# Optimization experiments

Measured on AMD Instinct MI355X. Metric: run time of the kernel, lower is better.

## Reference

```python
import jax, jax.numpy as jnp
import numpy as np

B, S, T, H, V = 32, 64, 64, 512, 32000


def setup_inputs() -> dict:
    key = jax.random.key(0)
    ks = jax.random.split(key, 14)
    enc = jax.random.normal(ks[0], (B, S, H), jnp.float32)
    h0 = jax.random.normal(ks[1], (1, B, H), jnp.float32)
    # encoder padding mask: at least half of each row valid (avoids all -inf rows)
    src_len = jax.random.randint(ks[2], (B,), S // 2, S + 1)
    enc_mask = (jnp.arange(S)[None, :] < src_len[:, None])
    tgt = jax.random.randint(ks[3], (B, T), 0, V)
    fra_len = jax.random.randint(ks[4], (B,), 1, T + 1).at[0].set(T)
    s = 1.0 / np.sqrt(H)
    emb = jax.random.normal(ks[5], (V, H), jnp.float32) * s
    W_ih = jax.random.uniform(ks[6], (3 * H, H), jnp.float32, -s, s)
    W_hh = jax.random.uniform(ks[7], (3 * H, H), jnp.float32, -s, s)
    b_ih = jax.random.uniform(ks[8], (3 * H,), jnp.float32, -s, s)
    b_hh = jax.random.uniform(ks[9], (3 * H,), jnp.float32, -s, s)
    W_cc = jax.random.uniform(ks[10], (H, 2 * H), jnp.float32, -s, s)
    b_cc = jnp.zeros((H,), jnp.float32)
    W_out = jax.random.uniform(ks[11], (V, H), jnp.float32, -s, s)
    b_out = jnp.zeros((V,), jnp.float32)
    return {"all_encoder_hidden_states": enc, "initial_decoder_hidden_state": h0,
            "encoder_output_mask": enc_mask, "target_input": tgt, "fra_length": fra_len,
            "embedding": emb, "W_ih": W_ih, "W_hh": W_hh, "b_ih": b_ih, "b_hh": b_hh,
            "W_cc": W_cc, "b_cc": b_cc, "W_out": W_out, "b_out": b_out}


def reference(all_encoder_hidden_states, initial_decoder_hidden_state, encoder_output_mask,
              target_input, fra_length, embedding, W_ih, W_hh, b_ih, b_hh,
              W_cc, b_cc, W_out, b_out):
    enc = all_encoder_hidden_states            # [B,S,H]
    mask = encoder_output_mask                 # [B,S] bool
    xs = embedding[target_input].transpose(1, 0, 2)  # [T,B,H]
    ts = jnp.arange(xs.shape[0])

    def step(h, inp):                          # h: [B,H]
        x, t = inp
        gx = x @ W_ih.T + b_ih                 # [B,3H]
        gh = h @ W_hh.T + b_hh
        gxr, gxz, gxn = jnp.split(gx, 3, axis=-1)
        ghr, ghz, ghn = jnp.split(gh, 3, axis=-1)
        r = jax.nn.sigmoid(gxr + ghr)
        z = jax.nn.sigmoid(gxz + ghz)
        n = jnp.tanh(gxn + r * ghn)
        h_new = (1.0 - z) * n + z * h          # torch GRU update
        # Luong dot-product attention
        scores = jnp.einsum('bsh,bh->bs', enc, h_new)
        scores = jnp.where(mask, scores, -jnp.inf)
        alphas = jax.nn.softmax(scores, axis=-1)
        ctx = jnp.einsum('bs,bsh->bh', alphas, enc)
        ho = jnp.tanh(jnp.concatenate([ctx, h_new], axis=-1) @ W_cc.T + b_cc)
        logit = ho @ W_out.T + b_out           # [B,V]
        active = (t < fra_length)[:, None]
        h_next = jnp.where(active, h_new, h)   # freeze finished sequences
        return h_next, logit

    _, logits = jax.lax.scan(step, initial_decoder_hidden_state[0], (xs, ts))
    logits = logits.transpose(1, 0, 2)          # [B,T,V]
    return jax.nn.log_softmax(logits, axis=-1)
```

## Files before the change

### kernel.cpp

```cpp
#include <hip/hip_runtime.h>

static constexpr int Bn = 32, Sn = 64, Tn = 64, Hn = 512, Vn = 32000;
static constexpr int H3 = 1536;

typedef __attribute__((ext_vector_type(8))) short bf16x8;
typedef __attribute__((ext_vector_type(4))) float f32x4;

__device__ __forceinline__ short f2bf(float f) {
    unsigned u = __float_as_uint(f);
    u += 0x7FFFu + ((u >> 16) & 1u);
    return (short)(u >> 16);
}
__device__ __forceinline__ float bf2f(short s) {
    return __uint_as_float(((unsigned)(unsigned short)s) << 16);
}

__device__ __forceinline__ void gload16(const void* g, void* l) {
    __builtin_amdgcn_global_load_lds(
        (const __attribute__((address_space(1))) unsigned int*)g,
        (__attribute__((address_space(3))) unsigned int*)l, 16, 0, 0);
}

__global__ __launch_bounds__(256) void k_prep(const int* __restrict__ tgt,
                                              const float* __restrict__ emb,
                                              const float* __restrict__ W_ih,
                                              const float* __restrict__ W_hh,
                                              const float* __restrict__ W_cc,
                                              short* __restrict__ Xb,
                                              short* __restrict__ Wih_b, short* __restrict__ Whh_b,
                                              short* __restrict__ Wc1_b, short* __restrict__ Wc2_b) {
    const int bid = blockIdx.x, tid = threadIdx.x;
    if (bid < 2048) {
        long u = (long)bid * 256 + tid;
        const float* src; short* dst;
        if (u < 196608)       { long e = u * 4;            src = W_ih + e; dst = Wih_b + e; }
        else if (u < 393216)  { long e = (u - 196608) * 4; src = W_hh + e; dst = Whh_b + e; }
        else if (u < 458752)  { long e = (u - 393216) * 4; long r = e >> 9; int c = (int)(e & 511);
                                src = W_cc + r * 1024 + c;       dst = Wc1_b + e; }
        else                  { long e = (u - 458752) * 4; long r = e >> 9; int c = (int)(e & 511);
                                src = W_cc + r * 1024 + 512 + c; dst = Wc2_b + e; }
        const float4 v = *(const float4*)src;
        short4 o; o.x = f2bf(v.x); o.y = f2bf(v.y); o.z = f2bf(v.z); o.w = f2bf(v.w);
        *(short4*)dst = o;
    } else {
        const int m = (bid - 2048) * 2 + (tid >> 7);
        const int c = (tid & 127) * 4;
        const float4 v = *(const float4*)(emb + (long)tgt[m] * Hn + c);
        short4 o; o.x = f2bf(v.x); o.y = f2bf(v.y); o.z = f2bf(v.z); o.w = f2bf(v.w);
        *(short4*)(Xb + (long)m * Hn + c) = o;
    }
}

__global__ __launch_bounds__(256) void k_gemm_bf16(const short* __restrict__ A, int lda,
                                                   const short* __restrict__ Bm, int ldb,
                                                   const float* __restrict__ bias,
                                                   float* __restrict__ C, int ldc, int K) {
    __shared__ short lA[4096];
    __shared__ short lB[4096];
    const int tid = threadIdx.x;
    const int row0 = blockIdx.y * 128;
    const int col0 = blockIdx.x * 128;
    const int lane = tid & 63;
    const int w = tid >> 6;
    const int wr = w >> 1, wc = w & 1;
    const int g = lane >> 4, rr = lane & 15;

    f32x4 acc[4][4];
    for (int m = 0; m < 4; ++m)
        for (int n = 0; n < 4; ++n)
            for (int q = 0; q < 4; ++q) acc[m][n][q] = 0.f;

    for (int kk = 0; kk < K; kk += 32) {
        for (int p = 0; p < 2; ++p) {
            int u = p * 256 + tid;
            int kg = u >> 7, r = u & 127;
            gload16(A + (long)(row0 + r) * lda + kk + kg * 8, &lA[u * 8]);
            gload16(Bm + (long)(col0 + r) * ldb + kk + kg * 8, &lB[u * 8]);
        }
        __syncthreads();
        bf16x8 av[4], bv[4];
        for (int m = 0; m < 4; ++m)
            av[m] = *(const bf16x8*)&lA[(g * 128 + wr * 64 + m * 16 + rr) * 8];
        for (int n = 0; n < 4; ++n)
            bv[n] = *(const bf16x8*)&lB[(g * 128 + wc * 64 + n * 16 + rr) * 8];
        for (int m = 0; m < 4; ++m)
            for (int n = 0; n < 4; ++n)
                acc[m][n] = __builtin_amdgcn_mfma_f32_16x16x32_bf16(av[m], bv[n], acc[m][n], 0, 0, 0);
        __syncthreads();
    }

    for (int n = 0; n < 4; ++n) {
        int gc = col0 + wc * 64 + n * 16 + rr;
        float bb = bias ? bias[gc] : 0.f;
        for (int m = 0; m < 4; ++m) {
            int gr = row0 + wr * 64 + m * 16 + g * 4;
            for (int q = 0; q < 4; ++q)
                C[(long)(gr + q) * ldc + gc] = acc[m][n][q] + bb;
        }
    }
}

__global__ __launch_bounds__(256) void k_gemm_logits(const short* __restrict__ A,
                                                     const short* __restrict__ Bm,
                                                     const float* __restrict__ bias,
                                                     float* __restrict__ Cf,
                                                     short* __restrict__ Cb,
                                                     float* __restrict__ stats,
                                                     int use_bf16) {
    __shared__ short lA[4096];
    __shared__ short lB[4096];
    __shared__ float sml[128][2];
    __shared__ float ssl[128][2];
    const int tid = threadIdx.x;
    const int row0 = blockIdx.y * 128;
    const int col0 = blockIdx.x * 128;
    const int lane = tid & 63;
    const int w = tid >> 6;
    const int wr = w >> 1, wc = w & 1;
    const int g = lane >> 4, rr = lane & 15;

    f32x4 acc[4][4];
    for (int m = 0; m < 4; ++m)
        for (int n = 0; n < 4; ++n)
            for (int q = 0; q < 4; ++q) acc[m][n][q] = 0.f;

    for (int kk = 0; kk < 512; kk += 32) {
        for (int p = 0; p < 2; ++p) {
            int u = p * 256 + tid;
            int kg = u >> 7, r = u & 127;
            gload16(A + (long)(row0 + r) * 512 + kk + kg * 8, &lA[u * 8]);
            gload16(Bm + (long)(col0 + r) * 512 + kk + kg * 8, &lB[u * 8]);
        }
        __syncthreads();
        bf16x8 av[4], bv[4];
        for (int m = 0; m < 4; ++m)
            av[m] = *(const bf16x8*)&lA[(g * 128 + wr * 64 + m * 16 + rr) * 8];
        for (int n = 0; n < 4; ++n)
            bv[n] = *(const bf16x8*)&lB[(g * 128 + wc * 64 + n * 16 + rr) * 8];
        for (int m = 0; m < 4; ++m)
            for (int n = 0; n < 4; ++n)
                acc[m][n] = __builtin_amdgcn_mfma_f32_16x16x32_bf16(av[m], bv[n], acc[m][n], 0, 0, 0);
        __syncthreads();
    }

    float bb[4];
    #pragma unroll
    for (int n = 0; n < 4; ++n) bb[n] = bias[col0 + wc * 64 + n * 16 + rr];

    if (use_bf16) {
        #pragma unroll
        for (int n = 0; n < 4; ++n) {
            int gc = col0 + wc * 64 + n * 16 + rr;
            #pragma unroll
            for (int m = 0; m < 4; ++m) {
                int gr = row0 + wr * 64 + m * 16 + g * 4;
                #pragma unroll
                for (int q = 0; q < 4; ++q)
                    Cb[(long)(gr + q) * Vn + gc] = f2bf(acc[m][n][q] + bb[n]);
            }
        }
    } else {
        #pragma unroll
        for (int n = 0; n < 4; ++n) {
            int gc = col0 + wc * 64 + n * 16 + rr;
            #pragma unroll
            for (int m = 0; m < 4; ++m) {
                int gr = row0 + wr * 64 + m * 16 + g * 4;
                #pragma unroll
                for (int q = 0; q < 4; ++q)
                    Cf[(long)(gr + q) * Vn + gc] = acc[m][n][q] + bb[n];
            }
        }
    }
    #pragma unroll
    for (int m = 0; m < 4; ++m) {
        #pragma unroll
        for (int q = 0; q < 4; ++q) {
            float mx = acc[m][0][q] + bb[0];
            mx = fmaxf(mx, acc[m][1][q] + bb[1]);
            mx = fmaxf(mx, acc[m][2][q] + bb[2]);
            mx = fmaxf(mx, acc[m][3][q] + bb[3]);
            mx = fmaxf(mx, __shfl_xor(mx, 1));
            mx = fmaxf(mx, __shfl_xor(mx, 2));
            mx = fmaxf(mx, __shfl_xor(mx, 4));
            mx = fmaxf(mx, __shfl_xor(mx, 8));
            float s = __expf(acc[m][0][q] + bb[0] - mx) + __expf(acc[m][1][q] + bb[1] - mx)
                    + __expf(acc[m][2][q] + bb[2] - mx) + __expf(acc[m][3][q] + bb[3] - mx);
            s += __shfl_xor(s, 1);
            s += __shfl_xor(s, 2);
            s += __shfl_xor(s, 4);
            s += __shfl_xor(s, 8);
            if (rr == 0) {
                const int r = wr * 64 + m * 16 + g * 4 + q;
                sml[r][wc] = mx; ssl[r][wc] = s;
            }
        }
    }
    __syncthreads();
    if (tid < 128) {
        const float m0 = sml[tid][0], m1 = sml[tid][1];
        const float mm = fmaxf(m0, m1);
        const float ss = ssl[tid][0] * __expf(m0 - mm) + ssl[tid][1] * __expf(m1 - mm);
        float2* sp = (float2*)stats;
        sp[(long)(row0 + tid) * 256 + blockIdx.x] = make_float2(mm, ss);
    }
}

__global__ __launch_bounds__(256) void k_sub(float* __restrict__ out, const short* __restrict__ Cb,
                                             const float* __restrict__ stats, int use_bf16) {
    const long row = blockIdx.x;
    const int tid = threadIdx.x;
    __shared__ float lse_s;
    if (tid < 64) {
        float m = -__builtin_inff(), s = 0.f;
        for (int tc = tid; tc < 250; tc += 64) {
            const float2 p = ((const float2*)stats)[row * 256 + tc];
            const float nm = fmaxf(m, p.x);
            s = s * __expf(m - nm) + p.y * __expf(p.x - nm);
            m = nm;
        }
        for (int o = 1; o < 64; o <<= 1) {
            const float om = __shfl_xor(m, o), os = __shfl_xor(s, o);
            const float nm = fmaxf(m, om);
            s = s * __expf(m - nm) + os * __expf(om - nm);
            m = nm;
        }
        if (tid == 0) lse_s = m + logf(s);
    }
    __syncthreads();
    const float lse = lse_s;
    float* p = out + row * (long)Vn;
    if (use_bf16) {
        const short* cp = Cb + row * (long)Vn;
        for (int i = tid; i < Vn / 4; i += 256) {
            short4 c = *(const short4*)(cp + i * 4);
            float4 v;
            v.x = bf2f(c.x) - lse; v.y = bf2f(c.y) - lse;
            v.z = bf2f(c.z) - lse; v.w = bf2f(c.w) - lse;
            *(float4*)(p + i * 4) = v;
        }
    } else {
        for (int i = tid; i < Vn / 4; i += 256) {
            float4 v = *(const float4*)(p + i * 4);
            v.x -= lse; v.y -= lse; v.z -= lse; v.w -= lse;
            *(float4*)(p + i * 4) = v;
        }
    }
}

__global__ __launch_bounds__(256) void k_ho(const short* __restrict__ A1, const short* __restrict__ A2,
                                            const short* __restrict__ B1, const short* __restrict__ B2,
                                            const float* __restrict__ bias, short* __restrict__ C) {
    __shared__ short lA[4096];
    __shared__ short lB[4096];
    const int tid = threadIdx.x;
    const int row0 = blockIdx.y * 128;
    const int col0 = blockIdx.x * 128;
    const int lane = tid & 63;
    const int w = tid >> 6;
    const int wr = w >> 1, wc = w & 1;
    const int g = lane >> 4, rr = lane & 15;

    f32x4 acc[4][4];
    for (int m = 0; m < 4; ++m)
        for (int n = 0; n < 4; ++n)
            for (int q = 0; q < 4; ++q) acc[m][n][q] = 0.f;

    for (int ph = 0; ph < 2; ++ph) {
        const short* A = ph ? A2 : A1;
        const short* Bm = ph ? B2 : B1;
        for (int kk = 0; kk < 512; kk += 32) {
            for (int p = 0; p < 2; ++p) {
                int u = p * 256 + tid;
                int kg = u >> 7, r = u & 127;
                gload16(A + (long)(row0 + r) * 512 + kk + kg * 8, &lA[u * 8]);
                gload16(Bm + (long)(col0 + r) * 512 + kk + kg * 8, &lB[u * 8]);
            }
            __syncthreads();
            bf16x8 av[4], bv[4];
            for (int m = 0; m < 4; ++m)
                av[m] = *(const bf16x8*)&lA[(g * 128 + wr * 64 + m * 16 + rr) * 8];
            for (int n = 0; n < 4; ++n)
                bv[n] = *(const bf16x8*)&lB[(g * 128 + wc * 64 + n * 16 + rr) * 8];
            for (int m = 0; m < 4; ++m)
                for (int n = 0; n < 4; ++n)
                    acc[m][n] = __builtin_amdgcn_mfma_f32_16x16x32_bf16(av[m], bv[n], acc[m][n], 0, 0, 0);
            __syncthreads();
        }
    }

    for (int n = 0; n < 4; ++n) {
        int gc = col0 + wc * 64 + n * 16 + rr;
        float bb = bias[gc];
        for (int m = 0; m < 4; ++m) {
            int gr = row0 + wr * 64 + m * 16 + g * 4;
            for (int q = 0; q < 4; ++q)
                C[(long)(gr + q) * 512 + gc] = f2bf(tanhf(acc[m][n][q] + bb));
        }
    }
}

__device__ __forceinline__ void sig_flag(unsigned* slot, unsigned val) {
    asm volatile("s_waitcnt vmcnt(0)" ::: "memory");
    __syncthreads();
    if (threadIdx.x == 0)
        __hip_atomic_store(slot, val, __ATOMIC_RELAXED, __HIP_MEMORY_SCOPE_AGENT);
}

__global__ __launch_bounds__(512, 1) void k_seq(
    const float* __restrict__ GX, const int* __restrict__ fra,
    const float* __restrict__ h0,
    const short* __restrict__ Whh_b, const float* __restrict__ b_hh,
    short* __restrict__ hn_all,
    unsigned long long* __restrict__ hn_pub,
    unsigned* __restrict__ flags,
    const float* __restrict__ W_out, short* __restrict__ Wout_b)
{
    __shared__ __align__(16) short h_all[Bn * Hn];
    __shared__ float gh_sl[3 * 16 * 32];
    const int bid = blockIdx.x;
    const int tid = threadIdx.x;

    if (bid >= Bn) {
        const long base = (long)(bid - Bn) * (512 * 16);
        #pragma unroll
        for (int it = 0; it < 16; ++it) {
            long i = base + it * 512 + tid;
            if (i < (long)Vn * Hn / 4) {
                const float4 v = *(const float4*)(W_out + i * 4);
                short4 o; o.x = f2bf(v.x); o.y = f2bf(v.y); o.z = f2bf(v.z); o.w = f2bf(v.w);
                *(short4*)(Wout_b + i * 4) = o;
            }
        }
        return;
    }

    const int wv = tid >> 6, lane = tid & 63;
    bf16x8 afr[16];
    if (wv < 6) {
        const int g = wv >> 1;
        const int row = g * 512 + bid * 16 + (lane & 15);
        #pragma unroll
        for (int k = 0; k < 16; ++k)
            afr[k] = *(const bf16x8*)(Whh_b + (long)row * 512 + k * 32 + (lane >> 4) * 8);
    }
    #pragma unroll
    for (int it = 0; it < 8; ++it) {
        const int idx2 = it * 512 + tid;
        const int b = idx2 >> 7, ci2 = idx2 & 127;
        const int j0 = ci2 * 4;
        const int soff = b * 512 + ((((ci2 >> 1)) ^ (b & 7)) << 3) + (ci2 & 1) * 4;
        const float4 v = *(const float4*)(h0 + b * 512 + j0);
        unsigned long long pk = (unsigned long long)(unsigned short)f2bf(v.x)
                              | ((unsigned long long)(unsigned short)f2bf(v.y) << 16)
                              | ((unsigned long long)(unsigned short)f2bf(v.z) << 32)
                              | ((unsigned long long)(unsigned short)f2bf(v.w) << 48);
        *(unsigned long long*)&h_all[soff] = pk;
    }

    const int eb = tid >> 4, jj = tid & 15;
    float h_carry = h0[eb * 512 + bid * 16 + jj];
    const int flen_e = fra[eb];
    const int jglob = bid * 16 + jj;
    const float bhr = b_hh[jglob];
    const float bhz = b_hh[512 + jglob];
    const float bhn = b_hh[1024 + jglob];

    const int ci2s = wv * 16 + (lane & 15);
    const unsigned* fp = flags + (ci2s >> 2) * 32;
    const int bbase = lane >> 4;

    for (int t = 0; t < Tn; ++t) {
        const long base = (long)(eb * Tn + t) * H3 + jglob;
        const float gxr = GX[base];
        const float gxz = GX[base + 512];
        const float gxn = GX[base + 1024];
        if (t >= 1) {
            while (__hip_atomic_load(fp, __ATOMIC_RELAXED, __HIP_MEMORY_SCOPE_AGENT) < (unsigned)t)
                __builtin_amdgcn_s_sleep(1);
            const unsigned long long* src = hn_pub + ((t - 1) & 1) * 4096;
            #pragma unroll
            for (int it = 0; it < 8; ++it) {
                const int b = bbase + it * 4;
                const unsigned long long v =
                    __hip_atomic_load(src + b * 128 + ci2s, __ATOMIC_RELAXED, __HIP_MEMORY_SCOPE_AGENT);
                const int soff = b * 512 + ((((ci2s >> 1)) ^ (b & 7)) << 3) + (ci2s & 1) * 4;
                *(unsigned long long*)&h_all[soff] = v;
            }
        }
        __syncthreads();
        if (wv < 6) {
            const int g = wv >> 1, n = wv & 1;
            const int bq = n * 16 + (lane & 15);
            f32x4 a0 = {0.f, 0.f, 0.f, 0.f}, a1 = {0.f, 0.f, 0.f, 0.f};
            #pragma unroll
            for (int k = 0; k < 8; ++k) {
                const int c0 = k * 4 + (lane >> 4);
                const int c1 = (k + 8) * 4 + (lane >> 4);
                bf16x8 b0 = *(const bf16x8*)&h_all[bq * 512 + ((c0 ^ (bq & 7)) << 3)];
                bf16x8 b1 = *(const bf16x8*)&h_all[bq * 512 + ((c1 ^ (bq & 7)) << 3)];
                a0 = __builtin_amdgcn_mfma_f32_16x16x32_bf16(afr[k], b0, a0, 0, 0, 0);
                a1 = __builtin_amdgcn_mfma_f32_16x16x32_bf16(afr[k + 8], b1, a1, 0, 0, 0);
            }
            const int r0 = (lane >> 4) * 4;
            #pragma unroll
            for (int q = 0; q < 4; ++q)
                gh_sl[g * 512 + (r0 + q) * 32 + bq] = a0[q] + a1[q];
        }
        __syncthreads();
        {
            const float ghr = gh_sl[jj * 32 + eb]          + bhr;
            const float ghz = gh_sl[512 + jj * 32 + eb]    + bhz;
            const float ghn = gh_sl[1024 + jj * 32 + eb]   + bhn;
            const float r = 1.f / (1.f + __expf(-(gxr + ghr)));
            const float z = 1.f / (1.f + __expf(-(gxz + ghz)));
            const float nn = tanhf(gxn + r * ghn);
            const float hv = (1.f - z) * nn + z * h_carry;
            h_carry = (t < flen_e) ? hv : h_carry;
            int w32 = (int)(unsigned short)f2bf(h_carry);
            int n1 = __shfl_down(w32, 1);
            int n2 = __shfl_down(w32, 2);
            int n3 = __shfl_down(w32, 3);
            if ((jj & 3) == 0) {
                unsigned long long pk = (unsigned long long)(unsigned)(w32 | (n1 << 16))
                                      | ((unsigned long long)(unsigned)(n2 | (n3 << 16)) << 32);
                __hip_atomic_store(hn_pub + (t & 1) * 4096 + eb * 128 + bid * 4 + (jj >> 2), pk,
                                   __ATOMIC_RELAXED, __HIP_MEMORY_SCOPE_AGENT);
            }
            sig_flag(flags + bid * 32, (unsigned)(t + 1));
            hn_all[(long)(eb * Tn + t) * Hn + jglob] = f2bf(hv);
        }
    }
}

__global__ __launch_bounds__(512, 1) void k_attn(
    const float* __restrict__ enc, const short* __restrict__ hn_all,
    const void* __restrict__ maskp, short* __restrict__ ctx_b)
{
    __shared__ __align__(16) short encl[64 * 536];
    __shared__ __align__(16) short hnlbuf[64 * 536];
    __shared__ __align__(16) float scl[64 * 64];
    __shared__ __align__(16) short albc[64 * 72];
    const int b = blockIdx.x;
    const int tid = threadIdx.x;
    const int wv = tid >> 6, lane = tid & 63;
    const int g = lane >> 4, rr = lane & 15;

    const unsigned w0 = ((const unsigned*)maskp)[0];
    const int mmode = (w0 == 1u) ? 0 : (w0 == 0x3F800000u ? 2 : 1);

    {
        const float* encb = enc + (long)b * (Sn * Hn);
        #pragma unroll
        for (int it = 0; it < 16; ++it) {
            int e = (it * 512 + tid) * 4;
            float4 v = *(const float4*)(encb + e);
            int s = e >> 9, k = e & 511;
            short4 o; o.x = f2bf(v.x); o.y = f2bf(v.y); o.z = f2bf(v.z); o.w = f2bf(v.w);
            *(short4*)(encl + s * 536 + k) = o;
        }
    }
    {
        const short* hb = hn_all + (long)b * (Tn * Hn);
        #pragma unroll
        for (int it = 0; it < 8; ++it) {
            int u = it * 512 + tid;
            int t = u >> 6, k8 = (u & 63) * 8;
            *(int4*)(hnlbuf + t * 536 + k8) = *(const int4*)(hb + t * 512 + k8);
        }
    }
    __syncthreads();

    for (int i = 0; i < 2; ++i) {
        const int id = wv * 2 + i;
        const int tt = id >> 2, ss = id & 3;
        f32x4 a0 = {0.f, 0.f, 0.f, 0.f}, a1 = {0.f, 0.f, 0.f, 0.f};
        #pragma unroll
        for (int k = 0; k < 8; ++k) {
            bf16x8 av0 = *(const bf16x8*)&hnlbuf[(tt * 16 + rr) * 536 + k * 32 + g * 8];
            bf16x8 bv0 = *(const bf16x8*)&encl[(ss * 16 + rr) * 536 + k * 32 + g * 8];
            bf16x8 av1 = *(const bf16x8*)&hnlbuf[(tt * 16 + rr) * 536 + (k + 8) * 32 + g * 8];
            bf16x8 bv1 = *(const bf16x8*)&encl[(ss * 16 + rr) * 536 + (k + 8) * 32 + g * 8];
            a0 = __builtin_amdgcn_mfma_f32_16x16x32_bf16(av0, bv0, a0, 0, 0, 0);
            a1 = __builtin_amdgcn_mfma_f32_16x16x32_bf16(av1, bv1, a1, 0, 0, 0);
        }
        #pragma unroll
        for (int q = 0; q < 4; ++q)
            scl[(tt * 16 + g * 4 + q) * 64 + ss * 16 + rr] = a0[q] + a1[q];
    }
    __syncthreads();

    {
        const int t = wv * 8 + (lane >> 3);
        const int sub = lane & 7;
        float v[8];
        #pragma unroll
        for (int e = 0; e < 8; ++e) {
            const int s = sub * 8 + e;
            bool mv;
            if (mmode == 0)      mv = ((const int*)maskp)[b * Sn + s] != 0;
            else if (mmode == 1) mv = ((const unsigned char*)maskp)[b * Sn + s] != 0;
            else                 mv = ((const float*)maskp)[b * Sn + s] != 0.f;
            v[e] = mv ? scl[t * 64 + s] : -__builtin_inff();
        }
        float mx = v[0];
        #pragma unroll
        for (int e = 1; e < 8; ++e) mx = fmaxf(mx, v[e]);
        mx = fmaxf(mx, __shfl_xor(mx, 1));
        mx = fmaxf(mx, __shfl_xor(mx, 2));
        mx = fmaxf(mx, __shfl_xor(mx, 4));
        float su = 0.f;
        float ev[8];
        #pragma unroll
        for (int e = 0; e < 8; ++e) { ev[e] = __expf(v[e] - mx); su += ev[e]; }
        su += __shfl_xor(su, 1);
        su += __shfl_xor(su, 2);
        su += __shfl_xor(su, 4);
        const float inv = 1.f / su;
        bf16x8 o;
        #pragma unroll
        for (int e = 0; e < 8; ++e) o[e] = f2bf(ev[e] * inv);
        *(bf16x8*)&albc[t * 72 + sub * 8] = o;
    }
    {
        short* enct = hnlbuf;
        const int j = tid;
        #pragma unroll
        for (int c = 0; c < 8; ++c) {
            bf16x8 tmp;
            #pragma unroll
            for (int e = 0; e < 8; ++e) tmp[e] = encl[(c * 8 + e) * 536 + j];
            *(bf16x8*)&enct[j * 64 + ((c ^ (j & 7)) * 8)] = tmp;
        }
    }
    __syncthreads();

    {
        const short* enct = hnlbuf;
        for (int i = 0; i < 16; ++i) {
            const int id = wv * 16 + i;
            const int tt = id >> 5, jt = id & 31;
            const int jr = jt * 16 + rr;
            f32x4 acc = {0.f, 0.f, 0.f, 0.f};
            #pragma unroll
            for (int kk = 0; kk < 2; ++kk) {
                bf16x8 av = *(const bf16x8*)&albc[(tt * 16 + rr) * 72 + kk * 32 + g * 8];
                const int c = kk * 4 + g;
                bf16x8 bv = *(const bf16x8*)&enct[jr * 64 + ((c ^ (jr & 7)) * 8)];
                acc = __builtin_amdgcn_mfma_f32_16x16x32_bf16(av, bv, acc, 0, 0, 0);
            }
            #pragma unroll
            for (int q = 0; q < 4; ++q) {
                const int t = tt * 16 + g * 4 + q;
                ctx_b[(long)(b * Tn + t) * Hn + jr] = f2bf(acc[q]);
            }
        }
    }
}

extern "C" void kernel_launch(void* const* d_in, const int* in_sizes, int n_in,
                              void* d_out, int out_size, void* d_ws, size_t ws_size,
                              hipStream_t stream) {
    const float* enc   = (const float*)d_in[0];
    const float* h0    = (const float*)d_in[1];
    const void*  maskp = d_in[2];
    const int*   tgt   = (const int*)d_in[3];
    const int*   fra   = (const int*)d_in[4];
    const float* emb   = (const float*)d_in[5];
    const float* W_ih  = (const float*)d_in[6];
    const float* W_hh  = (const float*)d_in[7];
    const float* b_ih  = (const float*)d_in[8];
    const float* b_hh  = (const float*)d_in[9];
    const float* W_cc  = (const float*)d_in[10];
    const float* b_cc  = (const float*)d_in[11];
    const float* W_out = (const float*)d_in[12];
    const float* b_out = (const float*)d_in[13];
    float* out = (float*)d_out;

    char* ws = (char*)d_ws;
    float*    GX      = (float*)ws;   ws += (long)2048 * 1536 * 4;
    short*    Xb      = (short*)ws;   ws += (long)2048 * 512 * 2;
    short*    Wih_b   = (short*)ws;   ws += (long)1536 * 512 * 2;
    short*    Wout_b  = (short*)ws;   ws += (long)32000 * 512 * 2;
    short*    Whh_b   = (short*)ws;   ws += (long)1536 * 512 * 2;
    short*    Wc1_b   = (short*)ws;   ws += (long)512 * 512 * 2;
    short*    Wcc2_b  = (short*)ws;   ws += (long)512 * 512 * 2;
    short*    ho_b    = (short*)ws;   ws += (long)2048 * 512 * 2;
    short*    hn_all  = (short*)ws;   ws += (long)2048 * 512 * 2;
    short*    ctx_b   = (short*)ws;   ws += (long)2048 * 512 * 2;
    float*    stats   = (float*)ws;   ws += (long)2048 * 256 * 2 * 4;
    unsigned long long* hn_pub = (unsigned long long*)ws; ws += (long)2 * 4096 * 8;
    unsigned* flags   = (unsigned*)ws; ws += 1024 * 4;
    const long cb_bytes = (long)2048 * Vn * 2;
    const long used = (long)(ws - (char*)d_ws);
    const int use_bf16 = (ws_size >= (size_t)(used + cb_bytes)) ? 1 : 0;
    short* Cb = use_bf16 ? (short*)ws : nullptr;

    hipMemsetAsync(flags, 0, 1024 * 4, stream);
    k_prep<<<3072, 256, 0, stream>>>(tgt, emb, W_ih, W_hh, W_cc, Xb, Wih_b, Whh_b, Wc1_b, Wcc2_b);

    k_gemm_bf16<<<dim3(12, 16), 256, 0, stream>>>(Xb, 512, Wih_b, 512, b_ih, GX, 1536, 512);

    k_seq<<<544, 512, 0, stream>>>(GX, fra, h0, Whh_b, b_hh, hn_all, hn_pub, flags, W_out, Wout_b);

    k_attn<<<32, 512, 0, stream>>>(enc, hn_all, maskp, ctx_b);

    k_ho<<<dim3(4, 16), 256, 0, stream>>>(ctx_b, hn_all, Wc1_b, Wcc2_b, b_cc, ho_b);

    k_gemm_logits<<<dim3(250, 16), 256, 0, stream>>>(ho_b, Wout_b, b_out, out, Cb, stats, use_bf16);

    k_sub<<<2048, 256, 0, stream>>>(out, Cb, stats, use_bf16);
}
```

Baseline: 675.1 us.

## Fuse attention into sequential GRU kernel via flag-driven consumer blocks

```diff
diff --git a/kernel.cpp b/kernel.cpp
--- a/kernel.cpp
+++ b/kernel.cpp
@@ -300,29 +300,49 @@
     }
 }
 
+struct WSm3 {
+    short h_all[Bn * Hn];
+    float gh_sl[3 * 16 * 32];
+};
+struct ASm3 {
+    short encl[Sn * 520];
+    float scp[8][64];
+    float al[64];
+    short hnf[Hn];
+};
+union USm3 { WSm3 w; ASm3 a; };
+
 __device__ __forceinline__ void sig_flag(unsigned* slot, unsigned val) {
     asm volatile("s_waitcnt vmcnt(0)" ::: "memory");
     __syncthreads();
     if (threadIdx.x == 0)
         __hip_atomic_store(slot, val, __ATOMIC_RELAXED, __HIP_MEMORY_SCOPE_AGENT);
 }
+__device__ __forceinline__ void wait_flags32(const unsigned* base, unsigned need) {
+    if (threadIdx.x < 32) {
+        while (__hip_atomic_load(base + threadIdx.x * 32, __ATOMIC_RELAXED, __HIP_MEMORY_SCOPE_AGENT) < need)
+            __builtin_amdgcn_s_sleep(1);
+    }
+    __syncthreads();
+}
 
 __global__ __launch_bounds__(512, 1) void k_seq(
     const float* __restrict__ GX, const int* __restrict__ fra,
     const float* __restrict__ h0,
     const short* __restrict__ Whh_b, const float* __restrict__ b_hh,
-    short* __restrict__ hn_all,
+    const float* __restrict__ enc, const void* __restrict__ maskp,
+    unsigned long long* __restrict__ hn_pk,
+    short* __restrict__ ctx_b,
     unsigned long long* __restrict__ hn_pub,
     unsigned* __restrict__ flags,
     const float* __restrict__ W_out, short* __restrict__ Wout_b)
 {
-    __shared__ __align__(16) short h_all[Bn * Hn];
-    __shared__ float gh_sl[3 * 16 * 32];
+    __shared__ __align__(16) USm3 sm;
     const int bid = blockIdx.x;
     const int tid = threadIdx.x;
 
-    if (bid >= Bn) {
-        const long base = (long)(bid - Bn) * (512 * 16);
+    if (bid >= 64) {
+        const long base = (long)(bid - 64) * (512 * 16);
         #pragma unroll
         for (int it = 0; it < 16; ++it) {
             long i = base + it * 512 + tid;
@@ -336,6 +356,75 @@
     }
 
     const int wv = tid >> 6, lane = tid & 63;
+
+    if (bid >= Bn) {
+        const int b = bid - Bn;
+        const unsigned w0 = ((const unsigned*)maskp)[0];
+        const int mmode = (w0 == 1u) ? 0 : (w0 == 0x3F800000u ? 2 : 1);
+        {
+            const float* encb = enc + (long)b * (Sn * Hn);
+            #pragma unroll
+            for (int it = 0; it < 16; ++it) {
+                int e = (it * 512 + tid) * 4;
+                float4 v = *(const float4*)(encb + e);
+                int s = e >> 9, k = e & 511;
+                short4 o; o.x = f2bf(v.x); o.y = f2bf(v.y); o.z = f2bf(v.z); o.w = f2bf(v.w);
+                *(short4*)(sm.a.encl + s * 520 + k) = o;
+            }
+        }
+        __syncthreads();
+        for (int u = 0; u < Tn; ++u) {
+            wait_flags32(flags, (unsigned)(u + 1));
+            if (tid < 128) {
+                unsigned long long v = __hip_atomic_load(hn_pk + (long)(b * Tn + u) * 128 + tid,
+                                                         __ATOMIC_RELAXED, __HIP_MEMORY_SCOPE_AGENT);
+                *(unsigned long long*)&sm.a.hnf[tid * 4] = v;
+            }
+            __syncthreads();
+            {
+                const int s = tid & 63, sub = tid >> 6;
+                const short* erow = sm.a.encl + s * 520 + sub * 64;
+                const short* hrow = sm.a.hnf + sub * 64;
+                float p = 0.f;
+                #pragma unroll
+                for (int c8 = 0; c8 < 8; ++c8) {
+                    bf16x8 ev = *(const bf16x8*)(erow + c8 * 8);
+                    bf16x8 hv8 = *(const bf16x8*)(hrow + c8 * 8);
+                    #pragma unroll
+                    for (int e = 0; e < 8; ++e)
+                        p += bf2f(ev[e]) * bf2f(hv8[e]);
+                }
+                sm.a.scp[sub][s] = p;
+            }
+            __syncthreads();
+            if (tid < 64) {
+                float v = 0.f;
+                #pragma unroll
+                for (int q = 0; q < 8; ++q) v += sm.a.scp[q][tid];
+                bool mv;
+                if (mmode == 0)      mv = ((const int*)maskp)[b * Sn + tid] != 0;
+                else if (mmode == 1) mv = ((const unsigned char*)maskp)[b * Sn + tid] != 0;
+                else                 mv = ((const float*)maskp)[b * Sn + tid] != 0.f;
+                v = mv ? v : -__builtin_inff();
+                float mx = v;
+                for (int o = 1; o < 64; o <<= 1) mx = fmaxf(mx, __shfl_xor(mx, o));
+                float e = __expf(v - mx);
+                float su = e;
+                for (int o = 1; o < 64; o <<= 1) su += __shfl_xor(su, o);
+                sm.a.al[tid] = e / su;
+            }
+            __syncthreads();
+            {
+                float cx = 0.f;
+                #pragma unroll 8
+                for (int s = 0; s < 64; ++s)
+                    cx += sm.a.al[s] * bf2f(sm.a.encl[s * 520 + tid]);
+                ctx_b[(long)(b * Tn + u) * Hn + tid] = f2bf(cx);
+            }
+        }
+        return;
+    }
+
     bf16x8 afr[16];
     if (wv < 6) {
         const int g = wv >> 1;
@@ -355,7 +444,7 @@
                               | ((unsigned long long)(unsigned short)f2bf(v.y) << 16)
                               | ((unsigned long long)(unsigned short)f2bf(v.z) << 32)
                               | ((unsigned long long)(unsigned short)f2bf(v.w) << 48);
-        *(unsigned long long*)&h_all[soff] = pk;
+        *(unsigned long long*)&sm.w.h_all[soff] = pk;
     }
 
     const int eb = tid >> 4, jj = tid & 15;
@@ -385,7 +474,7 @@
                 const unsigned long long v =
                     __hip_atomic_load(src + b * 128 + ci2s, __ATOMIC_RELAXED, __HIP_MEMORY_SCOPE_AGENT);
                 const int soff = b * 512 + ((((ci2s >> 1)) ^ (b & 7)) << 3) + (ci2s & 1) * 4;
-                *(unsigned long long*)&h_all[soff] = v;
+                *(unsigned long long*)&sm.w.h_all[soff] = v;
             }
         }
         __syncthreads();
@@ -397,163 +486,41 @@
             for (int k = 0; k < 8; ++k) {
                 const int c0 = k * 4 + (lane >> 4);
                 const int c1 = (k + 8) * 4 + (lane >> 4);
-                bf16x8 b0 = *(const bf16x8*)&h_all[bq * 512 + ((c0 ^ (bq & 7)) << 3)];
-                bf16x8 b1 = *(const bf16x8*)&h_all[bq * 512 + ((c1 ^ (bq & 7)) << 3)];
+                bf16x8 b0 = *(const bf16x8*)&sm.w.h_all[bq * 512 + ((c0 ^ (bq & 7)) << 3)];
+                bf16x8 b1 = *(const bf16x8*)&sm.w.h_all[bq * 512 + ((c1 ^ (bq & 7)) << 3)];
                 a0 = __builtin_amdgcn_mfma_f32_16x16x32_bf16(afr[k], b0, a0, 0, 0, 0);
                 a1 = __builtin_amdgcn_mfma_f32_16x16x32_bf16(afr[k + 8], b1, a1, 0, 0, 0);
             }
             const int r0 = (lane >> 4) * 4;
             #pragma unroll
             for (int q = 0; q < 4; ++q)
-                gh_sl[g * 512 + (r0 + q) * 32 + bq] = a0[q] + a1[q];
+                sm.w.gh_sl[g * 512 + (r0 + q) * 32 + bq] = a0[q] + a1[q];
         }
         __syncthreads();
         {
-            const float ghr = gh_sl[jj * 32 + eb]          + bhr;
-            const float ghz = gh_sl[512 + jj * 32 + eb]    + bhz;
-            const float ghn = gh_sl[1024 + jj * 32 + eb]   + bhn;
+            const float ghr = sm.w.gh_sl[jj * 32 + eb]          + bhr;
+            const float ghz = sm.w.gh_sl[512 + jj * 32 + eb]    + bhz;
+            const float ghn = sm.w.gh_sl[1024 + jj * 32 + eb]   + bhn;
             const float r = 1.f / (1.f + __expf(-(gxr + ghr)));
             const float z = 1.f / (1.f + __expf(-(gxz + ghz)));
             const float nn = tanhf(gxn + r * ghn);
             const float hv = (1.f - z) * nn + z * h_carry;
             h_carry = (t < flen_e) ? hv : h_carry;
-            int w32 = (int)(unsigned short)f2bf(h_carry);
-            int n1 = __shfl_down(w32, 1);
-            int n2 = __shfl_down(w32, 2);
-            int n3 = __shfl_down(w32, 3);
+            int f32w = (int)(unsigned short)f2bf(h_carry);
+            int r32w = (int)(unsigned short)f2bf(hv);
+            int f1 = __shfl_down(f32w, 1), f2 = __shfl_down(f32w, 2), f3 = __shfl_down(f32w, 3);
+            int r1 = __shfl_down(r32w, 1), r2 = __shfl_down(r32w, 2), r3 = __shfl_down(r32w, 3);
             if ((jj & 3) == 0) {
-                unsigned long long pk = (unsigned long long)(unsigned)(w32 | (n1 << 16))
-                                      | ((unsigned long long)(unsigned)(n2 | (n3 << 16)) << 32);
-                __hip_atomic_store(hn_pub + (t & 1) * 4096 + eb * 128 + bid * 4 + (jj >> 2), pk,
+                unsigned long long pkf = (unsigned long long)(unsigned)(f32w | (f1 << 16))
+                                       | ((unsigned long long)(unsigned)(f2 | (f3 << 16)) << 32);
+                unsigned long long pkr = (unsigned long long)(unsigned)(r32w | (r1 << 16))
+                                       | ((unsigned long long)(unsigned)(r2 | (r3 << 16)) << 32);
+                __hip_atomic_store(hn_pub + (t & 1) * 4096 + eb * 128 + bid * 4 + (jj >> 2), pkf,
                                    __ATOMIC_RELAXED, __HIP_MEMORY_SCOPE_AGENT);
+                __hip_atomic_store(hn_pk + (long)(eb * Tn + t) * 128 + bid * 4 + (jj >> 2), pkr,
+                                   __ATOMIC_RELAXED, __HIP_MEMORY_SCOPE_AGENT);
             }
             sig_flag(flags + bid * 32, (unsigned)(t + 1));
-            hn_all[(long)(eb * Tn + t) * Hn + jglob] = f2bf(hv);
-        }
-    }
-}
-
-__global__ __launch_bounds__(512, 1) void k_attn(
-    const float* __restrict__ enc, const short* __restrict__ hn_all,
-    const void* __restrict__ maskp, short* __restrict__ ctx_b)
-{
-    __shared__ __align__(16) short encl[64 * 536];
-    __shared__ __align__(16) short hnlbuf[64 * 536];
-    __shared__ __align__(16) float scl[64 * 64];
-    __shared__ __align__(16) short albc[64 * 72];
-    const int b = blockIdx.x;
-    const int tid = threadIdx.x;
-    const int wv = tid >> 6, lane = tid & 63;
-    const int g = lane >> 4, rr = lane & 15;
-
-    const unsigned w0 = ((const unsigned*)maskp)[0];
-    const int mmode = (w0 == 1u) ? 0 : (w0 == 0x3F800000u ? 2 : 1);
-
-    {
-        const float* encb = enc + (long)b * (Sn * Hn);
-        #pragma unroll
-        for (int it = 0; it < 16; ++it) {
-            int e = (it * 512 + tid) * 4;
-            float4 v = *(const float4*)(encb + e);
-            int s = e >> 9, k = e & 511;
-            short4 o; o.x = f2bf(v.x); o.y = f2bf(v.y); o.z = f2bf(v.z); o.w = f2bf(v.w);
-            *(short4*)(encl + s * 536 + k) = o;
-        }
-    }
-    {
-        const short* hb = hn_all + (long)b * (Tn * Hn);
-        #pragma unroll
-        for (int it = 0; it < 8; ++it) {
-            int u = it * 512 + tid;
-            int t = u >> 6, k8 = (u & 63) * 8;
-            *(int4*)(hnlbuf + t * 536 + k8) = *(const int4*)(hb + t * 512 + k8);
-        }
-    }
-    __syncthreads();
-
-    for (int i = 0; i < 2; ++i) {
-        const int id = wv * 2 + i;
-        const int tt = id >> 2, ss = id & 3;
-        f32x4 a0 = {0.f, 0.f, 0.f, 0.f}, a1 = {0.f, 0.f, 0.f, 0.f};
-        #pragma unroll
-        for (int k = 0; k < 8; ++k) {
-            bf16x8 av0 = *(const bf16x8*)&hnlbuf[(tt * 16 + rr) * 536 + k * 32 + g * 8];
-            bf16x8 bv0 = *(const bf16x8*)&encl[(ss * 16 + rr) * 536 + k * 32 + g * 8];
-            bf16x8 av1 = *(const bf16x8*)&hnlbuf[(tt * 16 + rr) * 536 + (k + 8) * 32 + g * 8];
-            bf16x8 bv1 = *(const bf16x8*)&encl[(ss * 16 + rr) * 536 + (k + 8) * 32 + g * 8];
-            a0 = __builtin_amdgcn_mfma_f32_16x16x32_bf16(av0, bv0, a0, 0, 0, 0);
-            a1 = __builtin_amdgcn_mfma_f32_16x16x32_bf16(av1, bv1, a1, 0, 0, 0);
-        }
-        #pragma unroll
-        for (int q = 0; q < 4; ++q)
-            scl[(tt * 16 + g * 4 + q) * 64 + ss * 16 + rr] = a0[q] + a1[q];
-    }
-    __syncthreads();
-
-    {
-        const int t = wv * 8 + (lane >> 3);
-        const int sub = lane & 7;
-        float v[8];
-        #pragma unroll
-        for (int e = 0; e < 8; ++e) {
-            const int s = sub * 8 + e;
-            bool mv;
-            if (mmode == 0)      mv = ((const int*)maskp)[b * Sn + s] != 0;
-            else if (mmode == 1) mv = ((const unsigned char*)maskp)[b * Sn + s] != 0;
-            else                 mv = ((const float*)maskp)[b * Sn + s] != 0.f;
-            v[e] = mv ? scl[t * 64 + s] : -__builtin_inff();
-        }
-        float mx = v[0];
-        #pragma unroll
-        for (int e = 1; e < 8; ++e) mx = fmaxf(mx, v[e]);
-        mx = fmaxf(mx, __shfl_xor(mx, 1));
-        mx = fmaxf(mx, __shfl_xor(mx, 2));
-        mx = fmaxf(mx, __shfl_xor(mx, 4));
-        float su = 0.f;
-        float ev[8];
-        #pragma unroll
-        for (int e = 0; e < 8; ++e) { ev[e] = __expf(v[e] - mx); su += ev[e]; }
-        su += __shfl_xor(su, 1);
-        su += __shfl_xor(su, 2);
-        su += __shfl_xor(su, 4);
-        const float inv = 1.f / su;
-        bf16x8 o;
-        #pragma unroll
-        for (int e = 0; e < 8; ++e) o[e] = f2bf(ev[e] * inv);
-        *(bf16x8*)&albc[t * 72 + sub * 8] = o;
-    }
-    {
-        short* enct = hnlbuf;
-        const int j = tid;
-        #pragma unroll
-        for (int c = 0; c < 8; ++c) {
-            bf16x8 tmp;
-            #pragma unroll
-            for (int e = 0; e < 8; ++e) tmp[e] = encl[(c * 8 + e) * 536 + j];
-            *(bf16x8*)&enct[j * 64 + ((c ^ (j & 7)) * 8)] = tmp;
-        }
-    }
-    __syncthreads();
-
-    {
-        const short* enct = hnlbuf;
-        for (int i = 0; i < 16; ++i) {
-            const int id = wv * 16 + i;
-            const int tt = id >> 5, jt = id & 31;
-            const int jr = jt * 16 + rr;
-            f32x4 acc = {0.f, 0.f, 0.f, 0.f};
-            #pragma unroll
-            for (int kk = 0; kk < 2; ++kk) {
-                bf16x8 av = *(const bf16x8*)&albc[(tt * 16 + rr) * 72 + kk * 32 + g * 8];
-                const int c = kk * 4 + g;
-                bf16x8 bv = *(const bf16x8*)&enct[jr * 64 + ((c ^ (jr & 7)) * 8)];
-                acc = __builtin_amdgcn_mfma_f32_16x16x32_bf16(av, bv, acc, 0, 0, 0);
-            }
-            #pragma unroll
-            for (int q = 0; q < 4; ++q) {
-                const int t = tt * 16 + g * 4 + q;
-                ctx_b[(long)(b * Tn + t) * Hn + jr] = f2bf(acc[q]);
-            }
         }
     }
 }
@@ -601,9 +568,9 @@
 
     k_gemm_bf16<<<dim3(12, 16), 256, 0, stream>>>(Xb, 512, Wih_b, 512, b_ih, GX, 1536, 512);
 
-    k_seq<<<544, 512, 0, stream>>>(GX, fra, h0, Whh_b, b_hh, hn_all, hn_pub, flags, W_out, Wout_b);
-
-    k_attn<<<32, 512, 0, stream>>>(enc, hn_all, maskp, ctx_b);
+    k_seq<<<576, 512, 0, stream>>>(GX, fra, h0, Whh_b, b_hh, enc, maskp,
+                                   (unsigned long long*)hn_all, ctx_b, hn_pub, flags,
+                                   W_out, Wout_b);
 
     k_ho<<<dim3(4, 16), 256, 0, stream>>>(ctx_b, hn_all, Wc1_b, Wcc2_b, b_cc, ho_b);
 
```

New measurement: 676.0 us. About the same (+0.1%).
